# Kernel tuning notes

Hardware: AMD Instinct MI355X
Metric: run time of the kernel (lower is better)

The kernel has to match this reference:

```python
import jax, jax.numpy as jnp
import numpy as np

B, SEQ_LEN, CHANNELS, PRED_LEN = 64, 1024, 512, 720
KERNEL = 25
PAD = (KERNEL - 1) // 2  # 12
IN_LEN = SEQ_LEN // 2    # 512
INV_SQRT2 = 1.0 / np.sqrt(2.0).astype(np.float32)


def dct2_ortho_matrix(N):
    # Orthonormal DCT-II basis: X_k = s_k * sum_n x_n cos(pi*(n+0.5)*k/N)
    n = np.arange(N, dtype=np.float64)
    k = np.arange(N, dtype=np.float64)
    M = np.cos(np.pi * (n[None, :] + 0.5) * k[:, None] / N)
    scale = np.sqrt(2.0 / N) * np.ones(N)
    scale[0] = np.sqrt(1.0 / N)
    return jnp.asarray((scale[:, None] * M).astype(np.float32))  # [k, n]


def setup_inputs() -> dict:
    key = jax.random.key(0)
    k1, k2, k3, k4, k5 = jax.random.split(key, 5)
    bound = 1.0 / np.sqrt(IN_LEN)
    return {
        "x": jax.random.normal(k1, (B, SEQ_LEN, CHANNELS), dtype=jnp.float32),
        "W_seasonal": jax.random.uniform(k2, (PRED_LEN, IN_LEN), jnp.float32, -bound, bound),
        "b_seasonal": jax.random.uniform(k3, (PRED_LEN,), jnp.float32, -bound, bound),
        "W_trend": jax.random.uniform(k4, (PRED_LEN, IN_LEN), jnp.float32, -bound, bound),
        "b_trend": jax.random.uniform(k5, (PRED_LEN,), jnp.float32, -bound, bound),
    }


def reference(x, W_seasonal, b_seasonal, W_trend, b_trend):
    # --- series decomposition: moving average (edge-padded, window 25) ---
    padded = jnp.pad(x, ((0, 0), (PAD, PAD), (0, 0)), mode="edge")  # [B, L+24, C]
    cs = jnp.cumsum(padded, axis=1)
    cs = jnp.pad(cs, ((0, 0), (1, 0), (0, 0)))  # leading zero, [B, L+25, C]
    trend = (cs[:, KERNEL:, :] - cs[:, :-KERNEL, :]) / KERNEL  # [B, L, C]
    seasonal = x - trend

    # [B, C, L]
    s = jnp.transpose(seasonal, (0, 2, 1))
    t = jnp.transpose(trend, (0, 2, 1))

    # --- grouped conv1d with [1,1]/sqrt(2), stride 2 (Haar low-pass downsample) ---
    def down(v):
        return (v[..., 0::2] + v[..., 1::2]) * INV_SQRT2  # [B, C, L/2]

    s = down(s)
    t = down(t)

    # --- orthonormal DCT-II over last axis, then divide by length ---
    Mdct = dct2_ortho_matrix(IN_LEN)  # [k, n]
    s = jnp.einsum("bcn,kn->bck", s, Mdct) / IN_LEN
    t = jnp.einsum("bcn,kn->bck", t, Mdct) / IN_LEN

    # --- shared Linear per branch ---
    s_out = jnp.einsum("bck,pk->bcp", s, W_seasonal) + b_seasonal
    t_out = jnp.einsum("bck,pk->bcp", t, W_trend) + b_trend

    out = s_out + t_out  # [B, C, pred_len]
    return jnp.transpose(out, (0, 2, 1))  # [B, pred_len, C]
```

## Files before the change

kernel.cpp:

```cpp
#include <hip/hip_runtime.h>
#include <hip/hip_bf16.h>
#include <math.h>


#define BATCH 64
#define SEQ 1024
#define CH 512
#define PRED 720
#define INV_SQRT2 0.70710678118654752440f

typedef __attribute__((ext_vector_type(4))) float floatx4;
typedef __attribute__((ext_vector_type(8))) short bf16x8;

#define KBF_OFF   0ull
#define BIAS_OFF  1572864ull
#define MW_OFF    1575936ull
#define WEFFS_OFF 2624512ull
#define WEFFT_OFF 4099072ull

__global__ void build_M(float* __restrict__ Mw) {
    int idx = blockIdx.x * 256 + threadIdx.x;
    int k = idx >> 9, n = idx & 511;
    int m = ((2 * n + 1) * k) & 2047;
    float ang = (float)m * (float)(M_PI / 1024.0);
    float scale = (k == 0) ? 0.04419417382415922f
                           : 0.0625f;
    Mw[idx] = cosf(ang) * scale * (1.0f / 512.0f);
}

__global__ void build_weff(const float* __restrict__ Ws_in, const float* __restrict__ Wt_in,
                           const float* __restrict__ Mw,
                           float* __restrict__ outS, float* __restrict__ outT) {
    const float* W = blockIdx.z ? Wt_in : Ws_in;
    float* out     = blockIdx.z ? outT  : outS;
    int n0 = blockIdx.x * 64;
    int p0 = blockIdx.y * 16;
    int t  = threadIdx.x;
    int tn = t & 63, tp = t >> 6;
    int pbase = p0 + tp * 4;
    __shared__ float mt[64][64];
    float a0 = 0.f, a1 = 0.f, a2 = 0.f, a3 = 0.f;
    for (int kb = 0; kb < 512; kb += 64) {
        __syncthreads();
        for (int i = 0; i < 16; i++) {
            int idx = t + i * 256;
            mt[idx >> 6][idx & 63] = Mw[(size_t)(kb + (idx >> 6)) * 512 + n0 + (idx & 63)];
        }
        __syncthreads();
        for (int kk = 0; kk < 64; kk++) {
            float m = mt[kk][tn];
            int kg = kb + kk;
            a0 += W[(size_t)(pbase + 0) * 512 + kg] * m;
            a1 += W[(size_t)(pbase + 1) * 512 + kg] * m;
            a2 += W[(size_t)(pbase + 2) * 512 + kg] * m;
            a3 += W[(size_t)(pbase + 3) * 512 + kg] * m;
        }
    }
    out[(size_t)(pbase + 0) * 512 + n0 + tn] = a0;
    out[(size_t)(pbase + 1) * 512 + n0 + tn] = a1;
    out[(size_t)(pbase + 2) * 512 + n0 + tn] = a2;
    out[(size_t)(pbase + 3) * 512 + n0 + tn] = a3;
}

__device__ __forceinline__ int tcnt(int j, int l) {
    if (l == 0)    return max(0, 13 - j);
    if (l == 1023) return max(0, j - 1010);
    int d = l - j; if (d < 0) d = -d;
    return (d <= 12) ? 1 : 0;
}

__global__ void build_kmat(const float* __restrict__ Ws, const float* __restrict__ Wt,
                           const float* __restrict__ bs, const float* __restrict__ bt,
                           __hip_bfloat16* __restrict__ Kbf, float* __restrict__ bias) {
    int idx = blockIdx.x * 256 + threadIdx.x;
    int p = idx >> 10, l = idx & 1023;
    if (p >= PRED) { Kbf[idx] = __float2bfloat16(0.0f); return; }
    if (l == 0) bias[p] = bs[p] + bt[p];
    float v = INV_SQRT2 * Ws[(size_t)p * 512 + (l >> 1)];
    int jlo = max(0, l - 12), jhi = min(1023, l + 12);
    float acc = 0.f;
    for (int n = (jlo >> 1); n <= (jhi >> 1); n++) {
        int c = tcnt(2 * n, l) + tcnt(2 * n + 1, l);
        if (c) acc += (Wt[(size_t)p * 512 + n] - Ws[(size_t)p * 512 + n]) * (float)c;
    }
    v += acc * (INV_SQRT2 / 25.0f);
    Kbf[idx] = __float2bfloat16(v);
}

__device__ __forceinline__ void async_ld16(const void* g, void* l) {
    __builtin_amdgcn_global_load_lds((const __attribute__((address_space(1))) void*)g,
                                     (__attribute__((address_space(3))) void*)l, 16, 0, 0);
}

__device__ __forceinline__ short f2bf(float f) {
    __hip_bfloat16 h = __float2bfloat16(f);
    return *reinterpret_cast<short*>(&h);
}

__global__ void __launch_bounds__(256) gemm_main(
    const short* __restrict__ Kbf, const float* __restrict__ x,
    const float* __restrict__ bias, float* __restrict__ out) {
    __shared__ __align__(16) short ldsA[128 * 32];
    int t = threadIdx.x;
    int wave = t >> 6, lane = t & 63;
    int mt = blockIdx.x % 6, nt = blockIdx.x / 6;
    int b  = blockIdx.y;
    int wm = wave >> 1, wn = wave & 1;
    const short* Ag = Kbf + (size_t)mt * 128 * 1024;
    const float* xb = x + (size_t)b * SEQ * CH;
    int lm = lane & 15, kq = lane >> 4;
    int cj[4];
    for (int j = 0; j < 4; j++) cj[j] = nt * 128 + wn * 64 + j * 16 + lm;

    floatx4 acc[4][4];
    for (int i = 0; i < 4; i++)
        for (int j = 0; j < 4; j++)
            acc[i][j] = (floatx4){0.f, 0.f, 0.f, 0.f};

    for (int k0 = 0; k0 < 1024; k0 += 32) {
        for (int rdi = 0; rdi < 2; rdi++) {
            int q = rdi * 256 + t;
            int row = q >> 2, ko = (q & 3) * 8;
            async_ld16(Ag + (size_t)row * 1024 + k0 + ko,
                       (char*)ldsA + rdi * 4096 + wave * 1024);
        }
        bf16x8 bfrag[4];
        int krow = k0 + kq * 8;
#pragma unroll
        for (int j = 0; j < 4; j++) {
            const float* xc = xb + (size_t)krow * CH + cj[j];
            bf16x8 bv;
#pragma unroll
            for (int i = 0; i < 8; i++) bv[i] = f2bf(xc[(size_t)i * CH]);
            bfrag[j] = bv;
        }
        __syncthreads();
        bf16x8 af[4];
        for (int i = 0; i < 4; i++)
            af[i] = *(const bf16x8*)&ldsA[(wm * 64 + i * 16 + lm) * 32 + kq * 8];
        for (int i = 0; i < 4; i++)
            for (int j = 0; j < 4; j++)
                acc[i][j] = __builtin_amdgcn_mfma_f32_16x16x32_bf16(af[i], bfrag[j], acc[i][j], 0, 0, 0);
        __syncthreads();
    }

    int p0 = mt * 128 + wm * 64;
    size_t outb = (size_t)b * PRED * CH;
    for (int i = 0; i < 4; i++) {
        for (int r = 0; r < 4; r++) {
            int p = p0 + i * 16 + kq * 4 + r;
            if (p < PRED) {
                float bv = bias[p];
                for (int j = 0; j < 4; j++) {
                    out[outb + (size_t)p * CH + cj[j]] = acc[i][j][r] + bv;
                }
            }
        }
    }
}

extern "C" void kernel_launch(void* const* d_in, const int* in_sizes, int n_in,
                              void* d_out, int out_size, void* d_ws, size_t ws_size,
                              hipStream_t stream) {
    const float* xp = nullptr; const float* wp[2] = {nullptr, nullptr};
    const float* bp[2] = {nullptr, nullptr};
    int wn = 0, bn = 0;
    for (int i = 0; i < n_in; i++) {
        if (in_sizes[i] == 33554432) xp = (const float*)d_in[i];
        else if (in_sizes[i] == 368640 && wn < 2) wp[wn++] = (const float*)d_in[i];
        else if (in_sizes[i] == 720 && bn < 2) bp[bn++] = (const float*)d_in[i];
    }
    if (!xp || wn != 2 || bn != 2) {
        xp = (const float*)d_in[0]; wp[0] = (const float*)d_in[1];
        bp[0] = (const float*)d_in[2]; wp[1] = (const float*)d_in[3];
        bp[1] = (const float*)d_in[4];
    }
    float* out = (float*)d_out;

    char* ws = (char*)d_ws;
    __hip_bfloat16* Kbf = (__hip_bfloat16*)(ws + KBF_OFF);
    float* bias  = (float*)(ws + BIAS_OFF);
    float* Mw    = (float*)(ws + MW_OFF);
    float* WeffS = (float*)(ws + WEFFS_OFF);
    float* WeffT = (float*)(ws + WEFFT_OFF);

    build_M<<<1024, 256, 0, stream>>>(Mw);
    build_weff<<<dim3(8, 45, 2), 256, 0, stream>>>(wp[0], wp[1], Mw, WeffS, WeffT);
    build_kmat<<<3072, 256, 0, stream>>>(WeffS, WeffT, bp[0], bp[1], Kbf, bias);
    gemm_main<<<dim3(24, 64), 256, 0, stream>>>((const short*)Kbf, xp, bias, out);
}
```

Measured before the change: 401.2 us.

## Pre-transpose x to bf16 channel-major and use vectorized-load GEMM with swizzled grid

Adds a transpose kernel that converts x to bf16 in [B, C, L] layout in workspace, so the GEMM can load B fragments as contiguous 16-byte vectors instead of eight strided fp32 loads with per-element conversion. The new GEMM also remaps block IDs for L2 locality, rearranges the LDS layout for A, and uses nontemporal output stores. build_weff caches W rows in shared memory. The cost is an extra full pass over x and a 64MB workspace, and the new path is used only when the workspace is large enough.

```diff
diff --git a/kernel.cpp b/kernel.cpp
--- a/kernel.cpp
+++ b/kernel.cpp
@@ -17,6 +17,8 @@
 #define MW_OFF    1575936ull
 #define WEFFS_OFF 2624512ull
 #define WEFFT_OFF 4099072ull
+#define XT_OFF    5573632ull
+#define WS_NEED   (XT_OFF + 67108864ull)
 
 __global__ void build_M(float* __restrict__ Mw) {
     int idx = blockIdx.x * 256 + threadIdx.x;
@@ -38,7 +40,15 @@
     int t  = threadIdx.x;
     int tn = t & 63, tp = t >> 6;
     int pbase = p0 + tp * 4;
+    __shared__ float wt[16][512];
     __shared__ float mt[64][64];
+#pragma unroll
+    for (int i = 0; i < 8; i++) {
+        int q = i * 256 + t;
+        int r = q >> 7, kq4 = q & 127;
+        floatx4 v = *reinterpret_cast<const floatx4*>(&W[(size_t)(p0 + r) * 512 + kq4 * 4]);
+        *reinterpret_cast<floatx4*>(&wt[r][kq4 * 4]) = v;
+    }
     float a0 = 0.f, a1 = 0.f, a2 = 0.f, a3 = 0.f;
     for (int kb = 0; kb < 512; kb += 64) {
         __syncthreads();
@@ -50,10 +60,10 @@
         for (int kk = 0; kk < 64; kk++) {
             float m = mt[kk][tn];
             int kg = kb + kk;
-            a0 += W[(size_t)(pbase + 0) * 512 + kg] * m;
-            a1 += W[(size_t)(pbase + 1) * 512 + kg] * m;
-            a2 += W[(size_t)(pbase + 2) * 512 + kg] * m;
-            a3 += W[(size_t)(pbase + 3) * 512 + kg] * m;
+            a0 += wt[tp * 4 + 0][kg] * m;
+            a1 += wt[tp * 4 + 1][kg] * m;
+            a2 += wt[tp * 4 + 2][kg] * m;
+            a3 += wt[tp * 4 + 3][kg] * m;
         }
     }
     out[(size_t)(pbase + 0) * 512 + n0 + tn] = a0;
@@ -95,6 +105,108 @@
 __device__ __forceinline__ short f2bf(float f) {
     __hip_bfloat16 h = __float2bfloat16(f);
     return *reinterpret_cast<short*>(&h);
+}
+
+__global__ void __launch_bounds__(256) xpose(const float* __restrict__ x,
+                                             short* __restrict__ xT) {
+    __shared__ float lds[64][65];
+    int t = threadIdx.x;
+    int l0 = blockIdx.x * 64, c0 = blockIdx.y * 64, b = blockIdx.z;
+    const float* xb = x + (size_t)b * SEQ * CH;
+    int row4 = t >> 4, cq = t & 15;
+#pragma unroll
+    for (int i = 0; i < 4; i++) {
+        int row = row4 + i * 16;
+        floatx4 v = *reinterpret_cast<const floatx4*>(
+            xb + (size_t)(l0 + row) * CH + c0 + cq * 4);
+#pragma unroll
+        for (int e = 0; e < 4; e++) lds[row][cq * 4 + e] = v[e];
+    }
+    __syncthreads();
+    size_t outb = (size_t)b * CH * SEQ;
+#pragma unroll
+    for (int r = 0; r < 2; r++) {
+        int u = r * 256 + t;
+        int lr = u & 7, c = u >> 3;
+        bf16x8 s;
+#pragma unroll
+        for (int e = 0; e < 8; e++) s[e] = f2bf(lds[lr * 8 + e][c]);
+        *reinterpret_cast<bf16x8*>(&xT[outb + (size_t)(c0 + c) * SEQ + l0 + lr * 8]) = s;
+    }
+}
+
+__global__ void __launch_bounds__(256) gemm_main_t(
+    const short* __restrict__ Kbf, const short* __restrict__ xT,
+    const float* __restrict__ bias, float* __restrict__ out) {
+    __shared__ __align__(16) short ldsA[128 * 32];
+    int t = threadIdx.x;
+    int wave = t >> 6, lane = t & 63;
+    int bid = blockIdx.x;
+    int work = (bid & 7) * 192 + (bid >> 3);
+    int mt = work % 6;
+    int grp = work / 6;
+    int nt = grp & 3, b = grp >> 2;
+    int wm = wave >> 1, wn = wave & 1;
+    int lm = lane & 15, kq = lane >> 4;
+    const short* Ag = Kbf + (size_t)mt * 128 * 1024;
+    const short* xrow[4];
+#pragma unroll
+    for (int j = 0; j < 4; j++) {
+        int c = nt * 128 + wn * 64 + j * 16 + lm;
+        xrow[j] = xT + ((size_t)b * CH + c) * 1024 + kq * 8;
+    }
+
+    floatx4 acc[4][4];
+#pragma unroll
+    for (int i = 0; i < 4; i++)
+#pragma unroll
+        for (int j = 0; j < 4; j++)
+            acc[i][j] = (floatx4){0.f, 0.f, 0.f, 0.f};
+
+    for (int k0 = 0; k0 < 1024; k0 += 32) {
+#pragma unroll
+        for (int rdi = 0; rdi < 2; rdi++) {
+            int q = rdi * 256 + t;
+            int row = ((q >> 6) << 4) + (q & 15);
+            int ko = ((q >> 4) & 3) * 8;
+            async_ld16(Ag + (size_t)row * 1024 + k0 + ko,
+                       (char*)ldsA + rdi * 4096 + wave * 1024);
+        }
+        bf16x8 bfrag[4];
+#pragma unroll
+        for (int j = 0; j < 4; j++)
+            bfrag[j] = *reinterpret_cast<const bf16x8*>(xrow[j] + k0);
+        __syncthreads();
+        bf16x8 af[4];
+#pragma unroll
+        for (int i = 0; i < 4; i++)
+            af[i] = *reinterpret_cast<const bf16x8*>(
+                (const char*)ldsA + ((wm * 4 + i) << 10) + (lane << 4));
+#pragma unroll
+        for (int i = 0; i < 4; i++)
+#pragma unroll
+            for (int j = 0; j < 4; j++)
+                acc[i][j] = __builtin_amdgcn_mfma_f32_16x16x32_bf16(af[i], bfrag[j], acc[i][j], 0, 0, 0);
+        __syncthreads();
+    }
+
+    int p0r = mt * 128 + wm * 64;
+    int cb = nt * 128 + wn * 64 + lm;
+    size_t outb = (size_t)b * PRED * CH;
+#pragma unroll
+    for (int i = 0; i < 4; i++) {
+#pragma unroll
+        for (int r = 0; r < 4; r++) {
+            int p = p0r + i * 16 + kq * 4 + r;
+            if (p < PRED) {
+                float bv = bias[p];
+#pragma unroll
+                for (int j = 0; j < 4; j++)
+                    __builtin_nontemporal_store(acc[i][j][r] + bv,
+                                                &out[outb + (size_t)p * CH + cb + j * 16]);
+            }
+        }
+    }
 }
 
 __global__ void __launch_bounds__(256) gemm_main(
@@ -183,9 +295,16 @@
     float* Mw    = (float*)(ws + MW_OFF);
     float* WeffS = (float*)(ws + WEFFS_OFF);
     float* WeffT = (float*)(ws + WEFFT_OFF);
-
+    short* xT    = (short*)(ws + XT_OFF);
+
+    bool big = (ws_size >= (size_t)WS_NEED);
+
+    if (big) xpose<<<dim3(16, 8, 64), 256, 0, stream>>>(xp, xT);
     build_M<<<1024, 256, 0, stream>>>(Mw);
     build_weff<<<dim3(8, 45, 2), 256, 0, stream>>>(wp[0], wp[1], Mw, WeffS, WeffT);
     build_kmat<<<3072, 256, 0, stream>>>(WeffS, WeffT, bp[0], bp[1], Kbf, bias);
-    gemm_main<<<dim3(24, 64), 256, 0, stream>>>((const short*)Kbf, xp, bias, out);
-}
+    if (big)
+        gemm_main_t<<<1536, 256, 0, stream>>>((const short*)Kbf, (const short*)xT, bias, out);
+    else
+        gemm_main<<<dim3(24, 64), 256, 0, stream>>>((const short*)Kbf, xp, bias, out);
+}
```

New measurement: 407.8 us. No clear change (+1.6%).
